# Kernel tuning notes

Measured on AMD Instinct MI355X. Metric: run time of the kernel, lower is better.

## Reference

```python
import jax, jax.numpy as jnp
import numpy as np

W = 0.5
EM_ITER = 5
SCALE = 20.0
N, T, D_IN, D_OUT, K, C1 = 16, 750, 2048, 2048, 8, 21  # C1 = class_num + 1


def l2n(f):
    # torch.norm(p=2, dim=-1, keepdim=True); divide with 1e-9 eps
    return f / (jnp.linalg.norm(f, axis=-1, keepdims=True) + 1e-9)


def setup_inputs() -> dict:
    key = jax.random.key(0)
    ks = jax.random.split(key, 5)
    x = jax.random.normal(ks[0], (N, T, D_IN), dtype=jnp.float32)
    W_emb = jax.random.normal(ks[1], (D_IN, D_OUT), dtype=jnp.float32) * (1.0 / np.sqrt(D_IN))
    b_emb = jnp.zeros((D_OUT,), dtype=jnp.float32)
    mu_param = jax.random.normal(ks[2], (K, D_OUT), dtype=jnp.float32) * 0.02
    ac_center = jax.random.normal(ks[3], (C1, D_OUT), dtype=jnp.float32) * 0.02
    fg_center = -1.0 * ac_center[-1][None, :]
    return {"x": x, "W_emb": W_emb, "b_emb": b_emb, "mu_param": mu_param,
            "ac_center": ac_center, "fg_center": fg_center}


def em(mu, x):
    norm_x = l2n(x)
    for _ in range(EM_ITER):
        norm_mu = l2n(mu)
        z = jax.nn.softmax(jnp.einsum('nkd,ntd->nkt', norm_mu, norm_x) * 5.0, axis=1)
        nz = z / (jnp.sum(z, axis=-1, keepdims=True) + 1e-9)
        mu = jnp.einsum('nkt,ntd->nkd', nz, x)
    return mu


def random_walk(x, y, w):
    n, t, _ = x.shape
    x_n, y_n = l2n(x), l2n(y)
    z = jax.nn.softmax(jnp.einsum('nkd,ntd->nkt', y_n, x_n) * 5.0, axis=1)  # (n,k,t)
    nz = z / (jnp.sum(z, axis=-1, keepdims=True) + 1e-9)
    affinity = jnp.einsum('nkt,nks->nts', z, nz)                             # (n,t,t)
    eye_t = jnp.eye(t, dtype=x.dtype)
    y2x_sum_x = w * jnp.einsum('nkt,nkd->ntd', z, y) + x
    # (I - w^2 A)^{-1} @ y2x_sum_x, expressed as a batched solve (same math as torch.solve)
    refined = (1.0 - w) * jnp.linalg.solve(eye_t[None] - (w * w) * affinity, y2x_sum_x)
    return refined


def prediction_module(x, ac_center, fg_center):
    nx = l2n(x)
    nac = l2n(ac_center)
    nfg = l2n(fg_center)
    frm_scrs = jnp.einsum('ntd,cd->ntc', nx, nac) * SCALE        # (n,t,C1)
    frm_fb = jnp.einsum('ntd,kd->ntk', nx, nfg)[..., 0] * SCALE  # (n,t)
    ca_att = jax.nn.sigmoid(frm_fb)
    cw_att = jax.nn.sigmoid(frm_scrs)
    ca_natt = ca_att / (jnp.sum(ca_att, axis=1, keepdims=True) + 1e-5)
    cw_natt = cw_att / (jnp.sum(cw_att, axis=1, keepdims=True) + 1e-5)
    ca_feat = jnp.einsum('ntd,nt->nd', x, ca_natt)
    cw_feat = jnp.einsum('ntd,ntc->ncd', x, cw_natt)
    ca_scr = jnp.einsum('nd,cd->nc', l2n(ca_feat), nac) * SCALE
    cw_scr = jnp.einsum('ncd,cd->nc', l2n(cw_feat), nac) * SCALE
    return (jax.nn.softmax(ca_scr, axis=-1), jax.nn.softmax(cw_scr, axis=-1), ca_att, frm_scrs)


def forward(x, W_emb, b_emb, mu_param, ac_center, fg_center):
    n = x.shape[0]
    x = jax.nn.relu(x @ W_emb + b_emb)  # feature_embedding (Dropout is identity in eval)
    mu = jnp.broadcast_to(mu_param[None], (n,) + mu_param.shape)
    mu = em(mu, x)
    reallocated_x = random_walk(x, mu, W)
    o_ca, o_cw, o_att, o_frm = prediction_module(x, ac_center, fg_center)
    m_ca, m_cw, m_att, m_frm = prediction_module(reallocated_x, ac_center, fg_center)
    mu_scr = jnp.einsum('nkd,cd->nkc', l2n(mu), l2n(ac_center)) * SCALE
    mu_pred = jax.nn.softmax(mu_scr, axis=-1)
    return (o_ca, o_cw, o_att, o_frm, m_ca, m_cw, m_att, m_frm, x, mu, mu_pred)


def reference(x, W_emb, b_emb, mu_param, ac_center, fg_center):
    return forward(x, W_emb, b_emb, mu_param, ac_center, fg_center)
```

## Files before the change

kernel.cpp:

```cpp
#include <hip/hip_runtime.h>

#define NB 16
#define TT 750
#define DD 2048
#define KK 8
#define CC 21
#define NT 12000

#define MU_CH 16
#define MU_TCH 47

typedef __bf16 bf16;
typedef __attribute__((ext_vector_type(4))) float floatx4;
typedef __attribute__((ext_vector_type(8))) __bf16 bf16x8;
typedef __attribute__((ext_vector_type(4))) __bf16 bf16x4;

__device__ __forceinline__ float wave_allreduce_sum(float v) {
#pragma unroll
  for (int m = 32; m > 0; m >>= 1) v += __shfl_xor(v, m, 64);
  return v;
}

__device__ __forceinline__ void async_lds16(const bf16* g, bf16* l) {
  __builtin_amdgcn_global_load_lds(
      (const __attribute__((address_space(1))) void*)(g),
      (__attribute__((address_space(3))) void*)(l), 16, 0, 0);
}

__global__ __launch_bounds__(256) void k_prep(
    const float* __restrict__ W, bf16* __restrict__ Wt,
    const float* __restrict__ ac, const float* __restrict__ fg,
    float* __restrict__ nacf, bf16* __restrict__ nacb,
    const float* __restrict__ mup, float* __restrict__ nmu, bf16* __restrict__ nmub,
    const float* __restrict__ x, bf16* __restrict__ Ab) {
  int b = blockIdx.x, tid = threadIdx.x;
  __shared__ float tile[32][33];
  __shared__ float sb[4];
  if (b < 4096) {
    int j0 = (b & 63) * 32, k0 = (b >> 6) * 32;
    int tx = tid & 31, ty = tid >> 5;
#pragma unroll
    for (int i = 0; i < 4; i++)
      tile[ty + 8 * i][tx] = W[(size_t)(k0 + ty + 8 * i) * DD + j0 + tx];
    __syncthreads();
#pragma unroll
    for (int i = 0; i < 4; i++)
      Wt[(size_t)(j0 + ty + 8 * i) * DD + k0 + tx] = (bf16)tile[tx][ty + 8 * i];
    return;
  }
  if (b < 4128) {
    int r = b - 4096;
    int d0 = tid * 8;
    if (r >= 22) {
#pragma unroll
      for (int j = 0; j < 8; j++) nacb[(size_t)r * DD + d0 + j] = (bf16)0.f;
      return;
    }
    const float* src = (r < 21) ? (ac + (size_t)r * DD) : fg;
    float v[8];
    floatx4 a = *(const floatx4*)(src + d0);
    floatx4 c = *(const floatx4*)(src + d0 + 4);
    v[0]=a.x; v[1]=a.y; v[2]=a.z; v[3]=a.w; v[4]=c.x; v[5]=c.y; v[6]=c.z; v[7]=c.w;
    float ss = 0.f;
#pragma unroll
    for (int j = 0; j < 8; j++) ss += v[j] * v[j];
    ss = wave_allreduce_sum(ss);
    int lane = tid & 63, wid = tid >> 6;
    if (lane == 0) sb[wid] = ss;
    __syncthreads();
    float inv = 1.f / (sqrtf(sb[0] + sb[1] + sb[2] + sb[3]) + 1e-9f);
#pragma unroll
    for (int j = 0; j < 8; j++) {
      float nv = v[j] * inv;
      nacf[(size_t)r * DD + d0 + j] = nv;
      nacb[(size_t)r * DD + d0 + j] = (bf16)nv;
    }
    return;
  }
  if (b < 4256) {
    int bb = b - 4128;
    int n = bb >> 3, k = bb & 7;
    int lane = tid & 63, wid = tid >> 6;
    const float* p = mup + (size_t)k * DD + tid * 8;
    float v[8];
    floatx4 a = *(const floatx4*)p;
    floatx4 c = *(const floatx4*)(p + 4);
    v[0]=a.x; v[1]=a.y; v[2]=a.z; v[3]=a.w; v[4]=c.x; v[5]=c.y; v[6]=c.z; v[7]=c.w;
    float ss = 0.f;
#pragma unroll
    for (int j = 0; j < 8; j++) ss += v[j] * v[j];
    ss = wave_allreduce_sum(ss);
    if (lane == 0) sb[wid] = ss;
    __syncthreads();
    float inv = 1.f / (sqrtf(sb[0] + sb[1] + sb[2] + sb[3]) + 1e-9f);
    float* q = nmu + (size_t)bb * DD + tid * 8;
    bf16* qb = nmub + (size_t)(n * 16 + k) * DD + tid * 8;
#pragma unroll
    for (int j = 0; j < 8; j++) {
      float nv = v[j] * inv;
      q[j] = nv;
      qb[j] = (bf16)nv;
    }
    return;
  }
  int unit0 = (b - 4256) * 4;
#pragma unroll
  for (int u = 0; u < 4; u++) {
    size_t base = ((size_t)(unit0 + u) * 256 + tid) * 8;
    int row = (int)(base >> 11);
    bf16x8 o = {};
    if (row < NT) {
      floatx4 a = *(const floatx4*)(x + base);
      floatx4 c = *(const floatx4*)(x + base + 4);
      o[0]=(bf16)a.x; o[1]=(bf16)a.y; o[2]=(bf16)a.z; o[3]=(bf16)a.w;
      o[4]=(bf16)c.x; o[5]=(bf16)c.y; o[6]=(bf16)c.z; o[7]=(bf16)c.w;
    }
    *(bf16x8*)(Ab + base) = o;
  }
}

__global__ __launch_bounds__(256) void k_gemm(
    const bf16* __restrict__ Ab, const bf16* __restrict__ Bt,
    const float* __restrict__ bias,
    float* __restrict__ Cout, bf16* __restrict__ Cb, float* __restrict__ rowsq) {
  __shared__ bf16 As[128 * 64];
  __shared__ bf16 Bs[128 * 64];
  int tid = threadIdx.x;
  int bid = blockIdx.x;
  int wid2 = (bid & 7) * 188 + (bid >> 3);
  int mt = wid2 >> 4, nt = wid2 & 15;
  int m0 = mt * 128, n0 = nt * 128;
  int wid = tid >> 6, lane = tid & 63;
  int wm = (wid >> 1) * 64, wn = (wid & 1) * 64;
  int lrow = lane & 15, lko = (lane >> 4) * 8;
  int lr7 = lrow & 7;
  floatx4 acc[4][4] = {};
  int crow = tid >> 3;
  int jg = ((tid & 7) ^ (crow & 7)) * 8;
  const bf16* gA = Ab + (size_t)(m0 + crow) * DD + jg;
  const bf16* gB = Bt + (size_t)(n0 + crow) * DD + jg;
  bf16* lA = As + tid * 8;
  bf16* lB = Bs + tid * 8;
  for (int k0 = 0; k0 < DD; k0 += 64) {
#pragma unroll
    for (int s = 0; s < 4; s++)
      async_lds16(gA + (size_t)(32 * s) * DD + k0, lA + 2048 * s);
#pragma unroll
    for (int s = 0; s < 4; s++)
      async_lds16(gB + (size_t)(32 * s) * DD + k0, lB + 2048 * s);
    __syncthreads();
#pragma unroll
    for (int ks = 0; ks < 64; ks += 32) {
      bf16x8 af[4], bfr[4];
#pragma unroll
      for (int i = 0; i < 4; i++) {
        int sw = (((ks + lko) >> 3) ^ lr7) * 8;
        af[i] = *(const bf16x8*)(As + (wm + i * 16 + lrow) * 64 + sw);
      }
#pragma unroll
      for (int jj = 0; jj < 4; jj++) {
        int sw = (((ks + lko) >> 3) ^ lr7) * 8;
        bfr[jj] = *(const bf16x8*)(Bs + (wn + jj * 16 + lrow) * 64 + sw);
      }
#pragma unroll
      for (int i = 0; i < 4; i++)
#pragma unroll
        for (int jj = 0; jj < 4; jj++)
          acc[i][jj] = __builtin_amdgcn_mfma_f32_16x16x32_bf16(af[i], bfr[jj], acc[i][jj], 0, 0, 0);
    }
    __syncthreads();
  }
  int quad = lane >> 4;
  float bv[4];
#pragma unroll
  for (int jj = 0; jj < 4; jj++) bv[jj] = bias[n0 + wn + jj * 16 + lrow];
#pragma unroll
  for (int i = 0; i < 4; i++) {
#pragma unroll
    for (int r = 0; r < 4; r++) {
      int row = m0 + wm + i * 16 + quad * 4 + r;
      bool ok = (row < NT);
      float sq = 0.f;
#pragma unroll
      for (int jj = 0; jj < 4; jj++) {
        int col = n0 + wn + jj * 16 + lrow;
        float v = acc[i][jj][r] + bv[jj];
        v = fmaxf(v, 0.f);
        if (ok) {
          Cout[(size_t)row * DD + col] = v;
          Cb[(size_t)row * DD + col] = (bf16)v;
        }
        sq += v * v;
      }
#pragma unroll
      for (int m = 1; m < 16; m <<= 1) sq += __shfl_xor(sq, m, 64);
      if (ok && lrow == 0) atomicAdd(&rowsq[row], sq);
    }
  }
}

__global__ __launch_bounds__(256) void k_score(
    const bf16* __restrict__ Xb, const bf16* __restrict__ nmub,
    const float* __restrict__ rowsq,
    float* __restrict__ z, float* __restrict__ rowsum) {
  __shared__ bf16 As[2][64 * 256];
  __shared__ bf16 Bs[2][16 * 256];
  int tid = threadIdx.x, lane = tid & 63, w = tid >> 6;
  int m0 = blockIdx.x * 64, n = blockIdx.y;
  int lrow = lane & 15, lko = (lane >> 4) * 8, lr7 = lrow & 7;
  int scg = tid & 31;
  int srow = tid >> 5;
  const bf16* gXn = Xb + (size_t)(n * TT + m0) * DD;
  const bf16* gBn = nmub + (size_t)(n * 16) * DD;
#pragma unroll
  for (int r = 0; r < 8; r++) {
    int row = r * 8 + srow;
    int cgg = (scg & 24) | ((scg & 7) ^ (row & 7));
    async_lds16(gXn + (size_t)row * DD + cgg * 8, &As[0][r * 2048 + tid * 8]);
  }
#pragma unroll
  for (int r = 0; r < 2; r++) {
    int row = r * 8 + srow;
    int cgg = (scg & 24) | ((scg & 7) ^ (row & 7));
    async_lds16(gBn + (size_t)row * DD + cgg * 8, &Bs[0][r * 2048 + tid * 8]);
  }
  floatx4 acc = {};
  int buf = 0;
  for (int k0 = 0; k0 < DD; k0 += 256) {
    __syncthreads();
    if (k0 + 256 < DD) {
#pragma unroll
      for (int r = 0; r < 8; r++) {
        int row = r * 8 + srow;
        int cgg = (scg & 24) | ((scg & 7) ^ (row & 7));
        async_lds16(gXn + (size_t)row * DD + k0 + 256 + cgg * 8,
                    &As[buf ^ 1][r * 2048 + tid * 8]);
      }
#pragma unroll
      for (int r = 0; r < 2; r++) {
        int row = r * 8 + srow;
        int cgg = (scg & 24) | ((scg & 7) ^ (row & 7));
        async_lds16(gBn + (size_t)row * DD + k0 + 256 + cgg * 8,
                    &Bs[buf ^ 1][r * 2048 + tid * 8]);
      }
    }
    int arow = w * 16 + lrow;
#pragma unroll
    for (int ks = 0; ks < 256; ks += 32) {
      int cg = (ks + lko) >> 3;
      int cgl = (cg & 24) | ((cg & 7) ^ lr7);
      bf16x8 a = *(const bf16x8*)(&As[buf][arow * 256 + cgl * 8]);
      bf16x8 b = *(const bf16x8*)(&Bs[buf][lrow * 256 + cgl * 8]);
      acc = __builtin_amdgcn_mfma_f32_16x16x32_bf16(a, b, acc, 0, 0, 0);
    }
    buf ^= 1;
  }
  int quad = lane >> 4;
  int k = lrow;
  float pacc = 0.f;
#pragma unroll
  for (int r = 0; r < 4; r++) {
    int trow = m0 + w * 16 + quad * 4 + r;
    bool valid = (trow < TT);
    float rq = valid ? rowsq[n * TT + trow] : 1.f;
    float s = acc[r] * (5.f / (sqrtf(rq) + 1e-9f));
    float mx = s;
    mx = fmaxf(mx, __shfl_xor(mx, 1, 64));
    mx = fmaxf(mx, __shfl_xor(mx, 2, 64));
    mx = fmaxf(mx, __shfl_xor(mx, 4, 64));
    float e = __expf(s - mx);
    float se = e;
    se += __shfl_xor(se, 1, 64);
    se += __shfl_xor(se, 2, 64);
    se += __shfl_xor(se, 4, 64);
    float zz = e / se;
    zz = (valid && k < 8) ? zz : 0.f;
    if (valid && k < 8) z[(size_t)(n * TT + trow) * 8 + k] = zz;
    pacc += zz;
  }
  pacc += __shfl_xor(pacc, 16, 64);
  pacc += __shfl_xor(pacc, 32, 64);
  if (lane < 8) atomicAdd(&rowsum[n * 8 + lane], pacc);
}

__global__ __launch_bounds__(256) void k_mu_accum(
    const bf16* __restrict__ Xb, const float* __restrict__ z,
    float* __restrict__ part2) {
  int n = blockIdx.x, tc = blockIdx.y, tid = threadIdx.x;
  int t0 = tc * MU_TCH;
  int tcnt = min(MU_TCH, TT - t0);
  __shared__ float zs[MU_TCH * 8];
  for (int i = tid; i < tcnt * 8; i += 256) zs[i] = z[(size_t)(n * TT + t0) * 8 + i];
  __syncthreads();
  float acc[8][8] = {};
  const bf16* xp = Xb + (size_t)(n * TT + t0) * DD + tid * 8;
  bf16x8 x0 = *(const bf16x8*)xp;
  bf16x8 x1 = (tcnt > 1) ? *(const bf16x8*)(xp + DD) : x0;
  for (int tt = 0; tt < tcnt; tt++) {
    bf16x8 cur = x0;
    x0 = x1;
    if (tt + 2 < tcnt) x1 = *(const bf16x8*)(xp + (size_t)(tt + 2) * DD);
    float xv[8];
#pragma unroll
    for (int j = 0; j < 8; j++) xv[j] = (float)cur[j];
    floatx4 za = *(const floatx4*)&zs[tt * 8];
    floatx4 zb4 = *(const floatx4*)&zs[tt * 8 + 4];
    float zk[8] = {za.x, za.y, za.z, za.w, zb4.x, zb4.y, zb4.z, zb4.w};
#pragma unroll
    for (int k = 0; k < 8; k++)
#pragma unroll
      for (int j = 0; j < 8; j++) acc[k][j] += zk[k] * xv[j];
  }
  float* pb = part2 + ((size_t)(tc * 16 + n) * 8) * DD + tid * 8;
#pragma unroll
  for (int k = 0; k < 8; k++) {
    floatx4 lo = {acc[k][0], acc[k][1], acc[k][2], acc[k][3]};
    floatx4 hi = {acc[k][4], acc[k][5], acc[k][6], acc[k][7]};
    *(floatx4*)(pb + (size_t)k * DD) = lo;
    *(floatx4*)(pb + (size_t)k * DD + 4) = hi;
  }
}

__global__ void k_mu_finish(const float* __restrict__ part2, const float* __restrict__ rs,
                            float* __restrict__ accS_raw, float* __restrict__ mu_ws,
                            float* __restrict__ mu_out, float* __restrict__ nmu_out,
                            bf16* __restrict__ nmub) {
  int b = blockIdx.x;
  int n = b >> 3, k = b & 7;
  int tid = threadIdx.x, lane = tid & 63, wid = tid >> 6;
  int d0 = tid * 8;
  float s[8] = {};
#pragma unroll 4
  for (int c = 0; c < MU_CH; c++) {
    const float* p = part2 + ((size_t)(c * 16 + n) * 8 + k) * DD + d0;
    floatx4 a = *(const floatx4*)p;
    floatx4 cc = *(const floatx4*)(p + 4);
    s[0] += a.x; s[1] += a.y; s[2] += a.z; s[3] += a.w;
    s[4] += cc.x; s[5] += cc.y; s[6] += cc.z; s[7] += cc.w;
  }
  if (accS_raw != nullptr) {
#pragma unroll
    for (int j = 0; j < 8; j++) accS_raw[(size_t)b * DD + d0 + j] = s[j];
    return;
  }
  float invr = 1.f / (rs[b] + 1e-9f);
  float m[8];
#pragma unroll
  for (int j = 0; j < 8; j++) m[j] = s[j] * invr;
#pragma unroll
  for (int j = 0; j < 8; j++) mu_ws[(size_t)b * DD + d0 + j] = m[j];
  if (mu_out != nullptr) {
#pragma unroll
    for (int j = 0; j < 8; j++) mu_out[(size_t)b * DD + d0 + j] = m[j];
  }
  float ss = 0.f;
#pragma unroll
  for (int j = 0; j < 8; j++) ss += m[j] * m[j];
  ss = wave_allreduce_sum(ss);
  __shared__ float sb[4];
  if (lane == 0) sb[wid] = ss;
  __syncthreads();
  float inv = 1.f / (sqrtf(sb[0] + sb[1] + sb[2] + sb[3]) + 1e-9f);
  bf16* qb = nmub + (size_t)(n * 16 + k) * DD + d0;
#pragma unroll
  for (int j = 0; j < 8; j++) {
    float nv = m[j] * inv;
    nmu_out[(size_t)b * DD + d0 + j] = nv;
    qb[j] = (bf16)nv;
  }
}

__global__ void k_wood_mupred(const float* __restrict__ z, const float* __restrict__ rowsum,
                              const float* __restrict__ S, const float* __restrict__ mu,
                              float* __restrict__ G,
                              const float* __restrict__ nmu, const float* __restrict__ nacf,
                              float* __restrict__ mupred) {
  int tid = threadIdx.x;
  if (blockIdx.x >= 16) {
    int b = blockIdx.x - 16;
    int lane = tid & 63, wid = tid >> 6;
    const float* v = nmu + (size_t)b * DD;
    __shared__ float scr[21];
    for (int c = wid; c < 21; c += 4) {
      const float* a = nacf + (size_t)c * DD;
      float s = 0.f;
      for (int i = lane * 4; i < DD; i += 256) {
        floatx4 vv = *(const floatx4*)(v + i);
        floatx4 aa = *(const floatx4*)(a + i);
        s += vv.x * aa.x + vv.y * aa.y + vv.z * aa.z + vv.w * aa.w;
      }
      s = wave_allreduce_sum(s);
      if (lane == 0) scr[c] = s * 20.f;
    }
    __syncthreads();
    if (tid == 0) {
      float mx = scr[0];
      for (int c = 1; c < 21; c++) mx = fmaxf(mx, scr[c]);
      float se = 0.f;
      for (int c = 0; c < 21; c++) se += __expf(scr[c] - mx);
      float inv = 1.f / se;
      for (int c = 0; c < 21; c++) mupred[(size_t)b * 21 + c] = __expf(scr[c] - mx) * inv;
    }
    return;
  }
  int n = blockIdx.x;
  __shared__ float VU[8][8];
  __shared__ float Mi[8][8];
  __shared__ float invrs[8];
  __shared__ float vus[64][4];
  if (tid < 8) invrs[tid] = 1.f / (rowsum[n * 8 + tid] + 1e-9f);
  {
    int pr = tid >> 2, sl = tid & 3;
    int jj = pr >> 3, kk = pr & 7;
    float s = 0.f;
    for (int t = sl; t < TT; t += 4) {
      const float* zp = z + (size_t)(n * TT + t) * 8;
      s += zp[jj] * zp[kk];
    }
    vus[pr][sl] = s;
  }
  __syncthreads();
  if (tid < 64)
    VU[tid >> 3][tid & 7] =
        (vus[tid][0] + vus[tid][1] + vus[tid][2] + vus[tid][3]) * invrs[tid >> 3];
  __syncthreads();
  if (tid == 0) {
    float M[8][16];
    for (int i = 0; i < 8; i++)
      for (int jj = 0; jj < 8; jj++) {
        M[i][jj] = ((i == jj) ? 1.f : 0.f) - 0.25f * VU[i][jj];
        M[i][8 + jj] = (i == jj) ? 1.f : 0.f;
      }
    for (int c = 0; c < 8; c++) {
      float pv = 1.f / M[c][c];
      for (int jj = 0; jj < 16; jj++) M[c][jj] *= pv;
      for (int rr = 0; rr < 8; rr++)
        if (rr != c) {
          float f = M[rr][c];
          for (int jj = 0; jj < 16; jj++) M[rr][jj] -= f * M[c][jj];
        }
    }
    for (int i = 0; i < 8; i++)
      for (int jj = 0; jj < 8; jj++) Mi[i][jj] = M[i][8 + jj];
  }
  __syncthreads();
  const float* mun = mu + (size_t)n * 8 * DD;
  const float* Sn = S + (size_t)n * 8 * DD;
  float* Gn = G + (size_t)n * 8 * DD;
  for (int d = tid; d < DD; d += 256) {
    float m[8], P[8];
#pragma unroll
    for (int k = 0; k < 8; k++) m[k] = mun[k * DD + d];
#pragma unroll
    for (int k = 0; k < 8; k++) {
      float s = 0.f;
#pragma unroll
      for (int jj = 0; jj < 8; jj++) s += VU[k][jj] * m[jj];
      P[k] = 0.5f * s + Sn[k * DD + d] * invrs[k];
    }
#pragma unroll
    for (int jj = 0; jj < 8; jj++) {
      float s = 0.f;
#pragma unroll
      for (int k = 0; k < 8; k++) s += Mi[jj][k] * P[k];
      Gn[jj * DD + d] = 0.5f * (0.5f * m[jj] + 0.25f * s);
    }
  }
}

__global__ __launch_bounds__(256) void k_rw_passC(
    const bf16* __restrict__ Xb, const float* __restrict__ z,
    const float* __restrict__ G, bf16* __restrict__ refb,
    float* __restrict__ invr) {
  int n = blockIdx.x, ch = blockIdx.y, tid = threadIdx.x;
  int lane = tid & 63, wid = tid >> 6;
  int d0 = tid * 8;
  int t0 = ch * 30;
  const float* Gn = G + (size_t)n * 8 * DD;
  float gr[8][8];
#pragma unroll
  for (int k = 0; k < 8; k++) {
    floatx4 a = *(const floatx4*)(Gn + k * DD + d0);
    floatx4 b = *(const floatx4*)(Gn + k * DD + d0 + 4);
    gr[k][0]=a.x; gr[k][1]=a.y; gr[k][2]=a.z; gr[k][3]=a.w;
    gr[k][4]=b.x; gr[k][5]=b.y; gr[k][6]=b.z; gr[k][7]=b.w;
  }
  __shared__ float red[30][4];
  const bf16* xrow = Xb + (size_t)n * TT * DD;
  bf16x8 xg = *(const bf16x8*)(xrow + (size_t)t0 * DD + d0);
  for (int tt = 0; tt < 30; tt++) {
    int t = t0 + tt;
    bf16x8 x8 = xg;
    if (tt + 1 < 30) xg = *(const bf16x8*)(xrow + (size_t)(t + 1) * DD + d0);
    const float* zp = z + (size_t)(n * TT + t) * 8;
    floatx4 za = *(const floatx4*)zp;
    floatx4 zb4 = *(const floatx4*)(zp + 4);
    float zt[8] = {za.x, za.y, za.z, za.w, zb4.x, zb4.y, zb4.z, zb4.w};
    float r[8];
#pragma unroll
    for (int j = 0; j < 8; j++) {
      float s = 0.5f * (float)x8[j];
#pragma unroll
      for (int k = 0; k < 8; k++) s += zt[k] * gr[k][j];
      r[j] = s;
    }
    bf16x8 ro;
#pragma unroll
    for (int j = 0; j < 8; j++) ro[j] = (bf16)r[j];
    *(bf16x8*)(refb + (size_t)(n * TT + t) * DD + d0) = ro;
    float ss = 0.f;
#pragma unroll
    for (int j = 0; j < 8; j++) ss += r[j] * r[j];
    ss = wave_allreduce_sum(ss);
    if (lane == 0) red[tt][wid] = ss;
  }
  __syncthreads();
  if (tid < 30) {
    float tot = red[tid][0] + red[tid][1] + red[tid][2] + red[tid][3];
    invr[n * TT + t0 + tid] = 1.f / (sqrtf(tot) + 1e-9f);
  }
}

__global__ __launch_bounds__(256) void k_pred_p1(
    const bf16* __restrict__ Xb, const bf16* __restrict__ nacb,
    const float* __restrict__ invn, int mode,
    float* __restrict__ out_frm, float* __restrict__ out_att,
    float* __restrict__ natt, float* __restrict__ att_sums) {
  __shared__ bf16 As[2][32 * 256];
  __shared__ bf16 Bs[2][32 * 256];
  __shared__ float ssum[2][32];
  int tid = threadIdx.x, lane = tid & 63, wid = tid >> 6;
  int m0 = blockIdx.x * 32;
  if (tid < 64) ssum[tid >> 5][tid & 31] = 0.f;
  int lrow = lane & 15, lko = (lane >> 4) * 8, lr7 = lrow & 7;
  int r0 = (wid & 1) * 16, c0 = (wid >> 1) * 16;
  int scg = tid & 31;
  int srow = tid >> 5;
  const bf16* gA = Xb + (size_t)m0 * DD;
  const bf16* gB = nacb;
#pragma unroll
  for (int r = 0; r < 4; r++) {
    int row = r * 8 + srow;
    int cgg = (scg & 24) | ((scg & 7) ^ (row & 7));
    async_lds16(gA + (size_t)row * DD + cgg * 8, &As[0][r * 2048 + tid * 8]);
    async_lds16(gB + (size_t)row * DD + cgg * 8, &Bs[0][r * 2048 + tid * 8]);
  }
  floatx4 acc = {};
  int buf = 0;
  for (int k0 = 0; k0 < DD; k0 += 256) {
    __syncthreads();
    if (k0 + 256 < DD) {
#pragma unroll
      for (int r = 0; r < 4; r++) {
        int row = r * 8 + srow;
        int cgg = (scg & 24) | ((scg & 7) ^ (row & 7));
        async_lds16(gA + (size_t)row * DD + k0 + 256 + cgg * 8,
                    &As[buf ^ 1][r * 2048 + tid * 8]);
        async_lds16(gB + (size_t)row * DD + k0 + 256 + cgg * 8,
                    &Bs[buf ^ 1][r * 2048 + tid * 8]);
      }
    }
#pragma unroll
    for (int ks = 0; ks < 256; ks += 32) {
      int cg = (ks + lko) >> 3;
      int cgl = (cg & 24) | ((cg & 7) ^ lr7);
      bf16x8 a = *(const bf16x8*)(&As[buf][(r0 + lrow) * 256 + cgl * 8]);
      bf16x8 b = *(const bf16x8*)(&Bs[buf][(c0 + lrow) * 256 + cgl * 8]);
      acc = __builtin_amdgcn_mfma_f32_16x16x32_bf16(a, b, acc, 0, 0, 0);
    }
    buf ^= 1;
  }
  __syncthreads();
  int quad = lane >> 4;
  int nbase = m0 / TT;
  int c = c0 + lrow;
#pragma unroll
  for (int r = 0; r < 4; r++) {
    int row = m0 + r0 + quad * 4 + r;
    if (c < 22) {
      float iv = mode ? (1.f / (sqrtf(invn[row]) + 1e-9f)) : invn[row];
      float s = acc[r] * iv * 20.f;
      float sg = 1.f / (1.f + __expf(-s));
      int n_loc = row / TT - nbase;
      if (c < 21) out_frm[(size_t)row * 21 + c] = s;
      else out_att[row] = sg;
      natt[(size_t)row * 22 + c] = sg;
      atomicAdd(&ssum[n_loc][c], sg);
    }
  }
  __syncthreads();
  if (tid < 64) {
    int nl = tid >> 5, cs = tid & 31;
    int nn = nbase + nl;
    if (cs < 22 && nn < NB) {
      float v = ssum[nl][cs];
      if (v != 0.f) atomicAdd(&att_sums[nn * 22 + cs], v);
    }
  }
}

__global__ __launch_bounds__(256) void k_pred_p2(
    const bf16* __restrict__ Xb, const float* __restrict__ natt,
    const float* __restrict__ sums, float* __restrict__ partF) {
  int n = blockIdx.x, dh = blockIdx.y, tc = blockIdx.z, tid = threadIdx.x;
  int d = dh * 1024 + tid * 4;
  int t0 = tc * 94;
  int tcnt = min(94, TT - t0);
  __shared__ float sw[94 * 22];
  for (int i = tid; i < tcnt * 22; i += 256) {
    int c = i - (i / 22) * 22;
    sw[i] = natt[(size_t)(n * TT + t0) * 22 + i] / (sums[n * 22 + c] + 1e-5f);
  }
  __syncthreads();
  float ac[22][4] = {};
  const bf16* xrow = Xb + (size_t)n * TT * DD;
  bf16x4 xg = *(const bf16x4*)(xrow + (size_t)t0 * DD + d);
  for (int tt = 0; tt < tcnt; tt++) {
    bf16x4 x4 = xg;
    if (tt + 1 < tcnt) xg = *(const bf16x4*)(xrow + (size_t)(t0 + tt + 1) * DD + d);
    float xv[4] = {(float)x4[0], (float)x4[1], (float)x4[2], (float)x4[3]};
#pragma unroll
    for (int cidx = 0; cidx < 22; cidx++) {
      float w = sw[tt * 22 + cidx];
#pragma unroll
      for (int jj = 0; jj < 4; jj++) ac[cidx][jj] += w * xv[jj];
    }
  }
  float* pb = partF + ((size_t)(n * 8 + tc) * 22) * DD + d;
#pragma unroll
  for (int cidx = 0; cidx < 22; cidx++) {
    floatx4 v = {ac[cidx][0], ac[cidx][1], ac[cidx][2], ac[cidx][3]};
    *(floatx4*)(pb + (size_t)cidx * DD) = v;
  }
}

__global__ void k_pred_final(const float* __restrict__ partF, float* __restrict__ feats,
                             const float* __restrict__ nacf,
                             float* __restrict__ oca, float* __restrict__ ocw) {
  int n = blockIdx.x, tid = threadIdx.x, lane = tid & 63, wid = tid >> 6;
  float* fnw = feats + (size_t)n * 22 * DD;
  const float* pp = partF + ((size_t)n * 8) * (22 * DD);
  for (int i = tid * 4; i < 22 * DD; i += 1024) {
    floatx4 s = {};
#pragma unroll
    for (int tc = 0; tc < 8; tc++) {
      floatx4 v = *(const floatx4*)(pp + (size_t)tc * 22 * DD + i);
      s.x += v.x; s.y += v.y; s.z += v.z; s.w += v.w;
    }
    *(floatx4*)(fnw + i) = s;
  }
  __threadfence_block();
  __syncthreads();
  const float* fn = fnw;
  __shared__ float rnorm[22];
  __shared__ float scr[42];
  for (int r = wid; r < 22; r += 4) {
    const float* fv = fn + (size_t)r * DD;
    float s = 0.f;
    for (int i = lane * 4; i < DD; i += 256) {
      floatx4 v = *(const floatx4*)(fv + i);
      s += v.x * v.x + v.y * v.y + v.z * v.z + v.w * v.w;
    }
    s = wave_allreduce_sum(s);
    if (lane == 0) rnorm[r] = 1.f / (sqrtf(s) + 1e-9f);
  }
  __syncthreads();
  for (int idx = wid; idx < 42; idx += 4) {
    int c = (idx < 21) ? idx : (idx - 21);
    int fr = (idx < 21) ? c : 21;
    const float* fv = fn + (size_t)fr * DD;
    const float* av = nacf + (size_t)c * DD;
    float s = 0.f;
    for (int i = lane * 4; i < DD; i += 256) {
      floatx4 v = *(const floatx4*)(fv + i);
      floatx4 a = *(const floatx4*)(av + i);
      s += v.x * a.x + v.y * a.y + v.z * a.z + v.w * a.w;
    }
    s = wave_allreduce_sum(s);
    if (lane == 0) scr[idx] = s * 20.f * rnorm[fr];
  }
  __syncthreads();
  if (tid < 2) {
    int base = (tid == 0) ? 21 : 0;
    float* dst = ((tid == 0) ? oca : ocw) + (size_t)n * 21;
    float mx = scr[base];
    for (int c = 1; c < 21; c++) mx = fmaxf(mx, scr[base + c]);
    float se = 0.f;
    for (int c = 0; c < 21; c++) se += __expf(scr[base + c] - mx);
    float inv = 1.f / se;
    for (int c = 0; c < 21; c++) dst[c] = __expf(scr[base + c] - mx) * inv;
  }
}

extern "C" void kernel_launch(void* const* d_in, const int* in_sizes, int n_in,
                              void* d_out, int out_size, void* d_ws, size_t ws_size,
                              hipStream_t stream) {
  const float* x_in = (const float*)d_in[0];
  const float* W = (const float*)d_in[1];
  const float* bemb = (const float*)d_in[2];
  const float* mup = (const float*)d_in[3];
  const float* ac = (const float*)d_in[4];
  const float* fg = (const float*)d_in[5];
  float* out = (float*)d_out;

  char* ws = (char*)d_ws;
  bf16* Wt = (bf16*)ws;
  bf16* Xb = (bf16*)(ws + 8388608);
  bf16* Rb = (bf16*)(ws + 57671680);
  bf16* Ab = (bf16*)(ws + 106954752);
  float* part2 = (float*)(ws + 106954752);
  float* partF = (float*)(ws + 106954752);
  bf16* nacb = (bf16*)(ws + 156237824);
  float* f = (float*)(ws + 156368896);
  float* nacf = f;
  float* mu = nacf + 45056;
  float* nmu = mu + 262144;
  bf16* nmub = (bf16*)(nmu + 262144);
  float* accS = nmu + 262144 + 262144;
  float* G = accS + 262144;
  float* z = G + 262144;
  float* natt = z + 96000;
  float* feats = natt + 264000;
  float* invr = feats + 720896;
  float* rowsum = invr + 12032;
  float* asums_o = rowsum + 768;
  float* asums_m = asums_o + 352;
  float* rowsq = asums_m + 352;

  float* o_ca = out;
  float* o_cw = out + 336;
  float* o_att = out + 672;
  float* o_frm = out + 12672;
  float* m_ca = out + 264672;
  float* m_cw = out + 265008;
  float* m_att = out + 265344;
  float* m_frm = out + 277344;
  float* x_out = out + 529344;
  float* mu_out = out + 25105344;
  float* mup_out = out + 25367488;

  hipMemsetAsync(rowsum, 0, (768 + 352 + 352 + 12032) * sizeof(float), stream);
  hipMemsetAsync(nmub, 0, (size_t)NB * 16 * DD * sizeof(bf16), stream);
  k_prep<<<7264, 256, 0, stream>>>(W, Wt, ac, fg, nacf, nacb, mup, nmu, nmub, x_in, Ab);
  k_gemm<<<1504, 256, 0, stream>>>(Ab, Wt, bemb, x_out, Xb, rowsq);
  for (int it = 0; it < 5; it++) {
    bool last = (it == 4);
    k_score<<<dim3(12, 16), 256, 0, stream>>>(Xb, nmub, rowsq, z, rowsum + it * 128);
    k_mu_accum<<<dim3(16, MU_CH), 256, 0, stream>>>(Xb, z, part2);
    k_mu_finish<<<128, 256, 0, stream>>>(part2, rowsum + it * 128, nullptr, mu,
                                         last ? mu_out : nullptr, nmu, nmub);
  }
  k_score<<<dim3(12, 16), 256, 0, stream>>>(Xb, nmub, rowsq, z, rowsum + 5 * 128);
  k_mu_accum<<<dim3(16, MU_CH), 256, 0, stream>>>(Xb, z, part2);
  k_mu_finish<<<128, 256, 0, stream>>>(part2, nullptr, accS, nullptr, nullptr, nullptr, nullptr);
  k_wood_mupred<<<144, 256, 0, stream>>>(z, rowsum + 5 * 128, accS, mu, G, nmu, nacf, mup_out);
  k_rw_passC<<<dim3(16, 25), 256, 0, stream>>>(Xb, z, G, Rb, invr);
  k_pred_p1<<<375, 256, 0, stream>>>(Xb, nacb, rowsq, 1, o_frm, o_att, natt, asums_o);
  k_pred_p2<<<dim3(16, 2, 8), 256, 0, stream>>>(Xb, natt, asums_o, partF);
  k_pred_final<<<16, 256, 0, stream>>>(partF, feats, nacf, o_ca, o_cw);
  k_pred_p1<<<375, 256, 0, stream>>>(Rb, nacb, invr, 0, m_frm, m_att, natt, asums_m);
  k_pred_p2<<<dim3(16, 2, 8), 256, 0, stream>>>(Rb, natt, asums_m, partF);
  k_pred_final<<<16, 256, 0, stream>>>(partF, feats, nacf, m_ca, m_cw);
}
```

Measured before the change: 875.9 us.

## Fuse EM score and mu accumulation into one kernel; coarsen pred_p2 chunks

Merges k_score and k_mu_accum into k_em_iter. After computing the softmax responsibilities for its 64-row tile, each block keeps them in shared memory and immediately accumulates that tile's weighted X into the mu partials. This removes one launch per EM iteration and the global round trip of z before accumulation. The trade-off is fewer, longer accumulation blocks (12 t-chunks instead of 16). The last tile also reads rows past T=750, beyond the batch and past the buffer end for n=15. Those reads are weighted by zero, but they are out of bounds and would produce NaN if the garbage decodes as NaN or Inf. Separately, k_pred_p2 now uses 4 larger t-chunks instead of 8, halving its grid and the partial-sum reduction work.

```diff
diff --git a/kernel.cpp b/kernel.cpp
--- a/kernel.cpp
+++ b/kernel.cpp
@@ -7,8 +7,9 @@
 #define CC 21
 #define NT 12000
 
-#define MU_CH 16
-#define MU_TCH 47
+#define EM_CH 12
+#define PF_CH 4
+#define PF_TCH 188
 
 typedef __bf16 bf16;
 typedef __attribute__((ext_vector_type(4))) float floatx4;
@@ -199,12 +200,13 @@
   }
 }
 
-__global__ __launch_bounds__(256) void k_score(
+__global__ __launch_bounds__(256) void k_em_iter(
     const bf16* __restrict__ Xb, const bf16* __restrict__ nmub,
     const float* __restrict__ rowsq,
-    float* __restrict__ z, float* __restrict__ rowsum) {
+    float* __restrict__ z, float* __restrict__ rowsum, float* __restrict__ part2) {
   __shared__ bf16 As[2][64 * 256];
   __shared__ bf16 Bs[2][16 * 256];
+  __shared__ float zs[64 * 8];
   int tid = threadIdx.x, lane = tid & 63, w = tid >> 6;
   int m0 = blockIdx.x * 64, n = blockIdx.y;
   int lrow = lane & 15, lko = (lane >> 4) * 8, lr7 = lrow & 7;
@@ -260,7 +262,8 @@
   float pacc = 0.f;
 #pragma unroll
   for (int r = 0; r < 4; r++) {
-    int trow = m0 + w * 16 + quad * 4 + r;
+    int tl = w * 16 + quad * 4 + r;
+    int trow = m0 + tl;
     bool valid = (trow < TT);
     float rq = valid ? rowsq[n * TT + trow] : 1.f;
     float s = acc[r] * (5.f / (sqrtf(rq) + 1e-9f));
@@ -275,31 +278,24 @@
     se += __shfl_xor(se, 4, 64);
     float zz = e / se;
     zz = (valid && k < 8) ? zz : 0.f;
-    if (valid && k < 8) z[(size_t)(n * TT + trow) * 8 + k] = zz;
+    if (k < 8) {
+      if (valid) z[(size_t)(n * TT + trow) * 8 + k] = zz;
+      zs[tl * 8 + k] = zz;
+    }
     pacc += zz;
   }
   pacc += __shfl_xor(pacc, 16, 64);
   pacc += __shfl_xor(pacc, 32, 64);
   if (lane < 8) atomicAdd(&rowsum[n * 8 + lane], pacc);
-}
-
-__global__ __launch_bounds__(256) void k_mu_accum(
-    const bf16* __restrict__ Xb, const float* __restrict__ z,
-    float* __restrict__ part2) {
-  int n = blockIdx.x, tc = blockIdx.y, tid = threadIdx.x;
-  int t0 = tc * MU_TCH;
-  int tcnt = min(MU_TCH, TT - t0);
-  __shared__ float zs[MU_TCH * 8];
-  for (int i = tid; i < tcnt * 8; i += 256) zs[i] = z[(size_t)(n * TT + t0) * 8 + i];
-  __syncthreads();
-  float acc[8][8] = {};
-  const bf16* xp = Xb + (size_t)(n * TT + t0) * DD + tid * 8;
+  __syncthreads();
+  float acc2[8][8] = {};
+  const bf16* xp = Xb + (size_t)(n * TT + m0) * DD + tid * 8;
   bf16x8 x0 = *(const bf16x8*)xp;
-  bf16x8 x1 = (tcnt > 1) ? *(const bf16x8*)(xp + DD) : x0;
-  for (int tt = 0; tt < tcnt; tt++) {
+  bf16x8 x1 = *(const bf16x8*)(xp + DD);
+  for (int tt = 0; tt < 64; tt++) {
     bf16x8 cur = x0;
     x0 = x1;
-    if (tt + 2 < tcnt) x1 = *(const bf16x8*)(xp + (size_t)(tt + 2) * DD);
+    if (tt + 2 < 64) x1 = *(const bf16x8*)(xp + (size_t)(tt + 2) * DD);
     float xv[8];
 #pragma unroll
     for (int j = 0; j < 8; j++) xv[j] = (float)cur[j];
@@ -307,17 +303,17 @@
     floatx4 zb4 = *(const floatx4*)&zs[tt * 8 + 4];
     float zk[8] = {za.x, za.y, za.z, za.w, zb4.x, zb4.y, zb4.z, zb4.w};
 #pragma unroll
-    for (int k = 0; k < 8; k++)
-#pragma unroll
-      for (int j = 0; j < 8; j++) acc[k][j] += zk[k] * xv[j];
-  }
-  float* pb = part2 + ((size_t)(tc * 16 + n) * 8) * DD + tid * 8;
-#pragma unroll
-  for (int k = 0; k < 8; k++) {
-    floatx4 lo = {acc[k][0], acc[k][1], acc[k][2], acc[k][3]};
-    floatx4 hi = {acc[k][4], acc[k][5], acc[k][6], acc[k][7]};
-    *(floatx4*)(pb + (size_t)k * DD) = lo;
-    *(floatx4*)(pb + (size_t)k * DD + 4) = hi;
+    for (int kk = 0; kk < 8; kk++)
+#pragma unroll
+      for (int j = 0; j < 8; j++) acc2[kk][j] += zk[kk] * xv[j];
+  }
+  float* pb = part2 + ((size_t)(blockIdx.x * 16 + n) * 8) * DD + tid * 8;
+#pragma unroll
+  for (int kk = 0; kk < 8; kk++) {
+    floatx4 lo = {acc2[kk][0], acc2[kk][1], acc2[kk][2], acc2[kk][3]};
+    floatx4 hi = {acc2[kk][4], acc2[kk][5], acc2[kk][6], acc2[kk][7]};
+    *(floatx4*)(pb + (size_t)kk * DD) = lo;
+    *(floatx4*)(pb + (size_t)kk * DD + 4) = hi;
   }
 }
 
@@ -331,7 +327,7 @@
   int d0 = tid * 8;
   float s[8] = {};
 #pragma unroll 4
-  for (int c = 0; c < MU_CH; c++) {
+  for (int c = 0; c < EM_CH; c++) {
     const float* p = part2 + ((size_t)(c * 16 + n) * 8 + k) * DD + d0;
     floatx4 a = *(const floatx4*)p;
     floatx4 cc = *(const floatx4*)(p + 4);
@@ -604,9 +600,9 @@
     const float* __restrict__ sums, float* __restrict__ partF) {
   int n = blockIdx.x, dh = blockIdx.y, tc = blockIdx.z, tid = threadIdx.x;
   int d = dh * 1024 + tid * 4;
-  int t0 = tc * 94;
-  int tcnt = min(94, TT - t0);
-  __shared__ float sw[94 * 22];
+  int t0 = tc * PF_TCH;
+  int tcnt = min(PF_TCH, TT - t0);
+  __shared__ float sw[PF_TCH * 22];
   for (int i = tid; i < tcnt * 22; i += 256) {
     int c = i - (i / 22) * 22;
     sw[i] = natt[(size_t)(n * TT + t0) * 22 + i] / (sums[n * 22 + c] + 1e-5f);
@@ -626,7 +622,7 @@
       for (int jj = 0; jj < 4; jj++) ac[cidx][jj] += w * xv[jj];
     }
   }
-  float* pb = partF + ((size_t)(n * 8 + tc) * 22) * DD + d;
+  float* pb = partF + ((size_t)(n * PF_CH + tc) * 22) * DD + d;
 #pragma unroll
   for (int cidx = 0; cidx < 22; cidx++) {
     floatx4 v = {ac[cidx][0], ac[cidx][1], ac[cidx][2], ac[cidx][3]};
@@ -639,11 +635,11 @@
                              float* __restrict__ oca, float* __restrict__ ocw) {
   int n = blockIdx.x, tid = threadIdx.x, lane = tid & 63, wid = tid >> 6;
   float* fnw = feats + (size_t)n * 22 * DD;
-  const float* pp = partF + ((size_t)n * 8) * (22 * DD);
+  const float* pp = partF + ((size_t)n * PF_CH) * (22 * DD);
   for (int i = tid * 4; i < 22 * DD; i += 1024) {
     floatx4 s = {};
 #pragma unroll
-    for (int tc = 0; tc < 8; tc++) {
+    for (int tc = 0; tc < PF_CH; tc++) {
       floatx4 v = *(const floatx4*)(pp + (size_t)tc * 22 * DD + i);
       s.x += v.x; s.y += v.y; s.z += v.z; s.w += v.w;
     }
@@ -745,20 +741,18 @@
   k_gemm<<<1504, 256, 0, stream>>>(Ab, Wt, bemb, x_out, Xb, rowsq);
   for (int it = 0; it < 5; it++) {
     bool last = (it == 4);
-    k_score<<<dim3(12, 16), 256, 0, stream>>>(Xb, nmub, rowsq, z, rowsum + it * 128);
-    k_mu_accum<<<dim3(16, MU_CH), 256, 0, stream>>>(Xb, z, part2);
+    k_em_iter<<<dim3(EM_CH, 16), 256, 0, stream>>>(Xb, nmub, rowsq, z, rowsum + it * 128, part2);
     k_mu_finish<<<128, 256, 0, stream>>>(part2, rowsum + it * 128, nullptr, mu,
                                          last ? mu_out : nullptr, nmu, nmub);
   }
-  k_score<<<dim3(12, 16), 256, 0, stream>>>(Xb, nmub, rowsq, z, rowsum + 5 * 128);
-  k_mu_accum<<<dim3(16, MU_CH), 256, 0, stream>>>(Xb, z, part2);
+  k_em_iter<<<dim3(EM_CH, 16), 256, 0, stream>>>(Xb, nmub, rowsq, z, rowsum + 5 * 128, part2);
   k_mu_finish<<<128, 256, 0, stream>>>(part2, nullptr, accS, nullptr, nullptr, nullptr, nullptr);
   k_wood_mupred<<<144, 256, 0, stream>>>(z, rowsum + 5 * 128, accS, mu, G, nmu, nacf, mup_out);
   k_rw_passC<<<dim3(16, 25), 256, 0, stream>>>(Xb, z, G, Rb, invr);
   k_pred_p1<<<375, 256, 0, stream>>>(Xb, nacb, rowsq, 1, o_frm, o_att, natt, asums_o);
-  k_pred_p2<<<dim3(16, 2, 8), 256, 0, stream>>>(Xb, natt, asums_o, partF);
+  k_pred_p2<<<dim3(16, 2, PF_CH), 256, 0, stream>>>(Xb, natt, asums_o, partF);
   k_pred_final<<<16, 256, 0, stream>>>(partF, feats, nacf, o_ca, o_cw);
   k_pred_p1<<<375, 256, 0, stream>>>(Rb, nacb, invr, 0, m_frm, m_att, natt, asums_m);
-  k_pred_p2<<<dim3(16, 2, 8), 256, 0, stream>>>(Rb, natt, asums_m, partF);
+  k_pred_p2<<<dim3(16, 2, PF_CH), 256, 0, stream>>>(Rb, natt, asums_m, partF);
   k_pred_final<<<16, 256, 0, stream>>>(partF, feats, nacf, m_ca, m_cw);
 }
```

After: 912.0 us. 1.04x slower.
